# Kernel tuning notes

Measured on AMD Instinct MI355X. Metric: run time of the kernel, lower is better.

The kernel has to match this reference:

```python
import jax, jax.numpy as jnp
import numpy as np

K = 512   # codebook entries per group (num_embeddings // 4)
D = 128   # dim per group (embedding_dim // 4)
BETA = 0.25


def setup_inputs() -> dict:
    key = jax.random.key(0)
    k0, k1, k2, k3, k4 = jax.random.split(key, 5)
    latents = jax.random.normal(k0, (16, 2048, 512), dtype=jnp.float32)
    scale = 1.0 / K
    w1 = jax.random.uniform(k1, (K, D), dtype=jnp.float32, minval=-scale, maxval=scale)
    w2 = jax.random.uniform(k2, (K, D), dtype=jnp.float32, minval=-scale, maxval=scale)
    w3 = jax.random.uniform(k3, (K, D), dtype=jnp.float32, minval=-scale, maxval=scale)
    w4 = jax.random.uniform(k4, (K, D), dtype=jnp.float32, minval=-scale, maxval=scale)
    return {"latents": latents, "w1": w1, "w2": w2, "w3": w3, "w4": w4}


def _vq(latents, w1, w2, w3, w4):
    B, S, E = latents.shape
    # Slicing [:, :, g*D:(g+1)*D] is equivalent to reshape into groups.
    x = latents.reshape(B, S, 4, D)                    # [B,S,4,D]
    W = jnp.stack([w1, w2, w3, w4], axis=0)            # [4,K,D]
    x_sq = jnp.sum(x * x, axis=-1, keepdims=True)      # [B,S,4,1]
    w_sq = jnp.sum(W * W, axis=-1)                     # [4,K]
    cross = jnp.einsum('bsgd,gkd->bsgk', x, W)         # [B,S,4,K]
    dist = x_sq + w_sq[None, None, :, :] - 2.0 * cross
    idx = jnp.argmin(dist, axis=-1)                    # [B,S,4]
    g_idx = jnp.arange(4)[None, None, :]
    q = W[g_idx, idx]                                  # [B,S,4,D]
    # per-group MSE losses (mean over B,S,D)
    sg = jax.lax.stop_gradient
    commit = jnp.mean((sg(q) - x) ** 2, axis=(0, 1, 3))   # [4]
    embed = jnp.mean((q - sg(x)) ** 2, axis=(0, 1, 3))    # [4]
    vq_loss = jnp.sum(BETA * commit + embed)
    # straight-through estimator
    q_st = x + sg(q - x)
    return q_st.reshape(B, S, E), vq_loss


def reference(latents, w1, w2, w3, w4):
    return _vq(latents, w1, w2, w3, w4)
```

## Files before the change

### kernel.cpp

```cpp
#include <hip/hip_runtime.h>
#include <stdint.h>

typedef __attribute__((ext_vector_type(8))) short short8;
typedef __attribute__((ext_vector_type(4))) float f32x4;

#define BIG 4.0f

static __device__ __forceinline__ short f2bf(float f) {
    union { float f; uint32_t u; } v; v.f = f;
    uint32_t u = v.u;
    return (short)((u + 0x7FFFu + ((u >> 16) & 1u)) >> 16);
}

__global__ __launch_bounds__(512, 2)
void vq_main_kernel(const float* __restrict__ lat,
                    const float* __restrict__ w0, const float* __restrict__ w1,
                    const float* __restrict__ w2, const float* __restrict__ w3,
                    float* __restrict__ out, float* __restrict__ ws) {
    __shared__ __align__(16) short lw[65536];
    __shared__ float lwsq[512];
    __shared__ float slsum[8];

    const int bid   = blockIdx.x;
    const int g     = bid >> 6;
    const int tbase = (bid & 63) * 512;
    const float* wg = (g == 0) ? w0 : (g == 1) ? w1 : (g == 2) ? w2 : w3;

    const int t    = threadIdx.x;
    const int wave = t >> 6;
    const int l    = t & 63;
    const int lr   = l & 15;
    const int lh   = l >> 4;
    const int col  = (l & 31) * 4;
    const uint32_t invlr = 511 - lr;

    {
        const int cl = l & 15;
        const int ub = l >> 4;
        #pragma unroll
        for (int p = 0; p < 4; p++) {
            int c   = p * 128 + wave * 16 + cl;
            int nt2 = c >> 4;
            const float* src = wg + (size_t)c * 128;
            float s = 0.f;
            #pragma unroll
            for (int sp = 0; sp < 4; sp++) {
                int u   = ub + sp * 4;
                int ks2 = u >> 2, lh2 = u & 3;
                float4 v0 = *(const float4*)(src + u * 8);
                float4 v1 = *(const float4*)(src + u * 8 + 4);
                s += v0.x*v0.x + v0.y*v0.y + v0.z*v0.z + v0.w*v0.w
                   + v1.x*v1.x + v1.y*v1.y + v1.z*v1.z + v1.w*v1.w;
                short8 b;
                b[0] = f2bf(v0.x); b[1] = f2bf(v0.y); b[2] = f2bf(v0.z); b[3] = f2bf(v0.w);
                b[4] = f2bf(v1.x); b[5] = f2bf(v1.y); b[6] = f2bf(v1.z); b[7] = f2bf(v1.w);
                *(short8*)((char*)lw +
                    (size_t)(((nt2 * 4 + ks2) * 64 + lh2 * 16 + cl) * 16)) = b;
            }
            s += __shfl_xor(s, 16);
            s += __shfl_xor(s, 32);
            if (ub == 0) lwsq[c] = BIG - 0.5f * s;
        }
    }

    const char* lwb = (const char*)lw + l * 16;
    const int wtok = tbase + wave * 64;

    auto load_convert = [&](short8 (&fr)[2][4], float (&xsp)[2], int wt) {
        #pragma unroll
        for (int mt = 0; mt < 2; mt++) {
            int token = wt + mt * 16 + lr;
            const float* xp = lat + (size_t)token * 512 + g * 128 + lh * 8;
            float part = 0.f;
            #pragma unroll
            for (int ks = 0; ks < 4; ks++) {
                float4 v0 = *(const float4*)(xp + ks * 32);
                float4 v1 = *(const float4*)(xp + ks * 32 + 4);
                part += v0.x*v0.x + v0.y*v0.y + v0.z*v0.z + v0.w*v0.w
                      + v1.x*v1.x + v1.y*v1.y + v1.z*v1.z + v1.w*v1.w;
                short8 a;
                a[0] = f2bf(v0.x); a[1] = f2bf(v0.y); a[2] = f2bf(v0.z); a[3] = f2bf(v0.w);
                a[4] = f2bf(v1.x); a[5] = f2bf(v1.y); a[6] = f2bf(v1.z); a[7] = f2bf(v1.w);
                fr[mt][ks] = a;
            }
            part += __shfl_xor(part, 16);
            part += __shfl_xor(part, 32);
            xsp[mt] = part;
        }
    };

    auto compute = [&](short8 (&af)[2][4], uint32_t (&rk)[8]) {
        short8 p0 = *(const short8*)(lwb);
        short8 p1 = *(const short8*)(lwb + 1024);
        short8 p2 = *(const short8*)(lwb + 2048);
        short8 p3 = *(const short8*)(lwb + 3072);
        float  ph = lwsq[lr];
        #pragma unroll 4
        for (int nt = 0; nt < 32; nt++) {
            short8 c0 = p0, c1 = p1, c2 = p2, c3 = p3;
            float  hn = ph;
            const char* nb = lwb + ((nt + 1) & 31) * 4096;
            p0 = *(const short8*)(nb);
            p1 = *(const short8*)(nb + 1024);
            p2 = *(const short8*)(nb + 2048);
            p3 = *(const short8*)(nb + 3072);
            ph = lwsq[(((nt + 1) & 31) << 4) + lr];
            const uint32_t invc = invlr - (uint32_t)(nt * 16);
            __builtin_amdgcn_s_setprio(1);
            f32x4 acc0 = {hn, hn, hn, hn};
            f32x4 acc1 = {hn, hn, hn, hn};
            acc0 = __builtin_amdgcn_mfma_f32_16x16x32_bf16(af[0][0], c0, acc0, 0, 0, 0);
            acc0 = __builtin_amdgcn_mfma_f32_16x16x32_bf16(af[0][1], c1, acc0, 0, 0, 0);
            acc0 = __builtin_amdgcn_mfma_f32_16x16x32_bf16(af[0][2], c2, acc0, 0, 0, 0);
            acc0 = __builtin_amdgcn_mfma_f32_16x16x32_bf16(af[0][3], c3, acc0, 0, 0, 0);
            acc1 = __builtin_amdgcn_mfma_f32_16x16x32_bf16(af[1][0], c0, acc1, 0, 0, 0);
            acc1 = __builtin_amdgcn_mfma_f32_16x16x32_bf16(af[1][1], c1, acc1, 0, 0, 0);
            acc1 = __builtin_amdgcn_mfma_f32_16x16x32_bf16(af[1][2], c2, acc1, 0, 0, 0);
            acc1 = __builtin_amdgcn_mfma_f32_16x16x32_bf16(af[1][3], c3, acc1, 0, 0, 0);
            __builtin_amdgcn_s_setprio(0);
            #pragma unroll
            for (int r = 0; r < 4; r++) {
                rk[r]     = max(rk[r],     (__float_as_uint(acc0[r]) & 0xFFFFFE00u) | invc);
                rk[4 + r] = max(rk[4 + r], (__float_as_uint(acc1[r]) & 0xFFFFFE00u) | invc);
            }
        }
    };

    auto epilogue = [&](uint32_t (&rk)[8], float (&xsp)[2], int wt, float& acc_lsum) {
        int runidx[8];
        #pragma unroll
        for (int i = 0; i < 8; i++) {
            uint32_t k = rk[i];
            k = max(k, (uint32_t)__shfl_xor((int)k, 1));
            k = max(k, (uint32_t)__shfl_xor((int)k, 2));
            k = max(k, (uint32_t)__shfl_xor((int)k, 4));
            k = max(k, (uint32_t)__shfl_xor((int)k, 8));
            rk[i] = k;
            runidx[i] = 511 - (int)(k & 0x1FFu);
        }
        #pragma unroll
        for (int mt = 0; mt < 2; mt++) {
            #pragma unroll
            for (int r = 0; r < 4; r++) {
                int row = lh * 4 + r;
                float xs = __shfl(xsp[mt], (l & 48) | row);
                float val = __uint_as_float(rk[mt * 4 + r] & 0xFFFFFE00u);
                if (lr == 0) acc_lsum += xs + 2.f * BIG - 2.f * val;
            }
        }
        #pragma unroll
        for (int it = 0; it < 16; it++) {
            const int j0 = it * 2, j1 = it * 2 + 1;
            int idx0 = __shfl(runidx[((j0 >> 4) << 2) | (j0 & 3)], ((j0 >> 2) & 3) << 4);
            int idx1 = __shfl(runidx[((j1 >> 4) << 2) | (j1 & 3)], ((j1 >> 2) & 3) << 4);
            int idx  = (l >= 32) ? idx1 : idx0;
            int tloc = it * 2 + (l >> 5);
            float4 v = *(const float4*)(wg + (size_t)idx * 128 + col);
            *(float4*)(out + (size_t)(wt + tloc) * 512 + g * 128 + col) = v;
        }
    };

    short8 fA[2][4], fB[2][4];
    float  xspA[2], xspB[2];
    uint32_t kA[8], kB[8];
    #pragma unroll
    for (int i = 0; i < 8; i++) { kA[i] = 0u; kB[i] = 0u; }

    load_convert(fA, xspA, wtok);
    __syncthreads();

    float lsum = 0.f;
    compute(fA, kA);

    float4 raw[16];
    #pragma unroll
    for (int mt = 0; mt < 2; mt++) {
        #pragma unroll
        for (int ks = 0; ks < 4; ks++) {
            const float* xp = lat + (size_t)(wtok + 32 + mt * 16 + lr) * 512
                            + g * 128 + lh * 8 + ks * 32;
            raw[mt * 8 + ks * 2]     = *(const float4*)(xp);
            raw[mt * 8 + ks * 2 + 1] = *(const float4*)(xp + 4);
        }
    }

    int runidxA[8];
    #pragma unroll
    for (int i = 0; i < 8; i++) {
        uint32_t k = kA[i];
        k = max(k, (uint32_t)__shfl_xor((int)k, 1));
        k = max(k, (uint32_t)__shfl_xor((int)k, 2));
        k = max(k, (uint32_t)__shfl_xor((int)k, 4));
        k = max(k, (uint32_t)__shfl_xor((int)k, 8));
        kA[i] = k;
        runidxA[i] = 511 - (int)(k & 0x1FFu);
    }
    #pragma unroll
    for (int mt = 0; mt < 2; mt++) {
        #pragma unroll
        for (int r = 0; r < 4; r++) {
            int row = lh * 4 + r;
            float xs = __shfl(xspA[mt], (l & 48) | row);
            float val = __uint_as_float(kA[mt * 4 + r] & 0xFFFFFE00u);
            if (lr == 0) lsum += xs + 2.f * BIG - 2.f * val;
        }
    }
    int widx[16];
    #pragma unroll
    for (int it = 0; it < 16; it++) {
        const int j0 = it * 2, j1 = it * 2 + 1;
        int idx0 = __shfl(runidxA[((j0 >> 4) << 2) | (j0 & 3)], ((j0 >> 2) & 3) << 4);
        int idx1 = __shfl(runidxA[((j1 >> 4) << 2) | (j1 & 3)], ((j1 >> 2) & 3) << 4);
        widx[it] = (l >= 32) ? idx1 : idx0;
    }

    #pragma unroll
    for (int mt = 0; mt < 2; mt++) {
        float part = 0.f;
        #pragma unroll
        for (int ks = 0; ks < 4; ks++) {
            float4 v0 = raw[mt * 8 + ks * 2];
            float4 v1 = raw[mt * 8 + ks * 2 + 1];
            part += v0.x*v0.x + v0.y*v0.y + v0.z*v0.z + v0.w*v0.w
                  + v1.x*v1.x + v1.y*v1.y + v1.z*v1.z + v1.w*v1.w;
            short8 a;
            a[0] = f2bf(v0.x); a[1] = f2bf(v0.y); a[2] = f2bf(v0.z); a[3] = f2bf(v0.w);
            a[4] = f2bf(v1.x); a[5] = f2bf(v1.y); a[6] = f2bf(v1.z); a[7] = f2bf(v1.w);
            fB[mt][ks] = a;
        }
        part += __shfl_xor(part, 16);
        part += __shfl_xor(part, 32);
        xspB[mt] = part;
    }

    {
        short8 p0 = *(const short8*)(lwb);
        short8 p1 = *(const short8*)(lwb + 1024);
        short8 p2 = *(const short8*)(lwb + 2048);
        short8 p3 = *(const short8*)(lwb + 3072);
        float  ph = lwsq[lr];
        float4 vb0, vb1;

#define FUSED_NT(nt)                                                           \
        {                                                                      \
            short8 c0 = p0, c1 = p1, c2 = p2, c3 = p3;                         \
            float  hn = ph;                                                    \
            const char* nb = lwb + (((nt) + 1) & 31) * 4096;                   \
            p0 = *(const short8*)(nb);                                         \
            p1 = *(const short8*)(nb + 1024);                                  \
            p2 = *(const short8*)(nb + 2048);                                  \
            p3 = *(const short8*)(nb + 3072);                                  \
            ph = lwsq[((((nt) + 1) & 31) << 4) + lr];                          \
            const uint32_t invc = invlr - (uint32_t)((nt) * 16);               \
            __builtin_amdgcn_s_setprio(1);                                     \
            f32x4 acc0 = {hn, hn, hn, hn};                                     \
            f32x4 acc1 = {hn, hn, hn, hn};                                     \
            acc0 = __builtin_amdgcn_mfma_f32_16x16x32_bf16(fB[0][0], c0, acc0, 0, 0, 0); \
            acc0 = __builtin_amdgcn_mfma_f32_16x16x32_bf16(fB[0][1], c1, acc0, 0, 0, 0); \
            acc0 = __builtin_amdgcn_mfma_f32_16x16x32_bf16(fB[0][2], c2, acc0, 0, 0, 0); \
            acc0 = __builtin_amdgcn_mfma_f32_16x16x32_bf16(fB[0][3], c3, acc0, 0, 0, 0); \
            acc1 = __builtin_amdgcn_mfma_f32_16x16x32_bf16(fB[1][0], c0, acc1, 0, 0, 0); \
            acc1 = __builtin_amdgcn_mfma_f32_16x16x32_bf16(fB[1][1], c1, acc1, 0, 0, 0); \
            acc1 = __builtin_amdgcn_mfma_f32_16x16x32_bf16(fB[1][2], c2, acc1, 0, 0, 0); \
            acc1 = __builtin_amdgcn_mfma_f32_16x16x32_bf16(fB[1][3], c3, acc1, 0, 0, 0); \
            __builtin_amdgcn_s_setprio(0);                                     \
            kB[0] = max(kB[0], (__float_as_uint(acc0[0]) & 0xFFFFFE00u) | invc); \
            kB[1] = max(kB[1], (__float_as_uint(acc0[1]) & 0xFFFFFE00u) | invc); \
            kB[2] = max(kB[2], (__float_as_uint(acc0[2]) & 0xFFFFFE00u) | invc); \
            kB[3] = max(kB[3], (__float_as_uint(acc0[3]) & 0xFFFFFE00u) | invc); \
            kB[4] = max(kB[4], (__float_as_uint(acc1[0]) & 0xFFFFFE00u) | invc); \
            kB[5] = max(kB[5], (__float_as_uint(acc1[1]) & 0xFFFFFE00u) | invc); \
            kB[6] = max(kB[6], (__float_as_uint(acc1[2]) & 0xFFFFFE00u) | invc); \
            kB[7] = max(kB[7], (__float_as_uint(acc1[3]) & 0xFFFFFE00u) | invc); \
            if (((nt) & 3) == 1) {                                             \
                const int it0 = ((nt) >> 2) * 2;                               \
                vb0 = *(const float4*)(wg + (size_t)widx[it0] * 128 + col);    \
                vb1 = *(const float4*)(wg + (size_t)widx[it0 + 1] * 128 + col);\
            }                                                                  \
            if (((nt) & 3) == 3) {                                             \
                const int it0 = ((nt) >> 2) * 2;                               \
                *(float4*)(out + (size_t)(wtok + it0 * 2 + (l >> 5)) * 512     \
                           + g * 128 + col) = vb0;                             \
                *(float4*)(out + (size_t)(wtok + (it0 + 1) * 2 + (l >> 5)) * 512 \
                           + g * 128 + col) = vb1;                             \
            }                                                                  \
        }
#define FUSED_4(n) FUSED_NT(n) FUSED_NT((n) + 1) FUSED_NT((n) + 2) FUSED_NT((n) + 3)
        FUSED_4(0)  FUSED_4(4)  FUSED_4(8)  FUSED_4(12)
        FUSED_4(16) FUSED_4(20) FUSED_4(24) FUSED_4(28)
#undef FUSED_4
#undef FUSED_NT
    }

    epilogue(kB, xspB, wtok + 32, lsum);

    lsum += __shfl_xor(lsum, 16);
    lsum += __shfl_xor(lsum, 32);
    if (l == 0) slsum[wave] = lsum;
    __syncthreads();
    if (t == 0) {
        float s = 0.f;
        #pragma unroll
        for (int i = 0; i < 8; i++) s += slsum[i];
        ws[4096 + bid] = s;
    }
}

__global__ void vq_finalize_kernel(const float* __restrict__ ws, float* __restrict__ out) {
    __shared__ float s4[4];
    float v = ws[4096 + threadIdx.x];
    #pragma unroll
    for (int m = 1; m < 64; m <<= 1) v += __shfl_xor(v, m);
    if ((threadIdx.x & 63) == 0) s4[threadIdx.x >> 6] = v;
    __syncthreads();
    if (threadIdx.x == 0)
        out[16777216] = 1.25f * (s4[0] + s4[1] + s4[2] + s4[3]) * (1.0f / 4194304.0f);
}

extern "C" void kernel_launch(void* const* d_in, const int* in_sizes, int n_in,
                              void* d_out, int out_size, void* d_ws, size_t ws_size,
                              hipStream_t stream) {
    const float* lat = (const float*)d_in[0];
    const float* w1  = (const float*)d_in[1];
    const float* w2  = (const float*)d_in[2];
    const float* w3  = (const float*)d_in[3];
    const float* w4  = (const float*)d_in[4];
    float* out = (float*)d_out;
    float* ws  = (float*)d_ws;

    vq_main_kernel<<<256, 512, 0, stream>>>(lat, w1, w2, w3, w4, out, ws);
    vq_finalize_kernel<<<1, 256, 0, stream>>>(ws, out);
}
```

Before: 40.48 us.

## Interleave next tile's first-half latent loads and bf16 conversion into first MFMA loop

Replaces the compute lambda for tile A with a fully unrolled macro loop that, every 8 codebook tiles, issues global loads for one k-slice of the next tile's first 16 rows and converts them to bf16 a few iterations later. Only the second 16-row half is still loaded after the loop. The aim is to hide global-load latency and conversion ALU work behind the MFMA stream instead of stalling between tiles. The cost is higher register pressure from full unrolling and the extra in-flight float4 registers, which could hurt occupancy under launch_bounds(512,2).

```diff
diff --git a/kernel.cpp b/kernel.cpp
--- a/kernel.cpp
+++ b/kernel.cpp
@@ -89,43 +89,6 @@
         }
     };
 
-    auto compute = [&](short8 (&af)[2][4], uint32_t (&rk)[8]) {
-        short8 p0 = *(const short8*)(lwb);
-        short8 p1 = *(const short8*)(lwb + 1024);
-        short8 p2 = *(const short8*)(lwb + 2048);
-        short8 p3 = *(const short8*)(lwb + 3072);
-        float  ph = lwsq[lr];
-        #pragma unroll 4
-        for (int nt = 0; nt < 32; nt++) {
-            short8 c0 = p0, c1 = p1, c2 = p2, c3 = p3;
-            float  hn = ph;
-            const char* nb = lwb + ((nt + 1) & 31) * 4096;
-            p0 = *(const short8*)(nb);
-            p1 = *(const short8*)(nb + 1024);
-            p2 = *(const short8*)(nb + 2048);
-            p3 = *(const short8*)(nb + 3072);
-            ph = lwsq[(((nt + 1) & 31) << 4) + lr];
-            const uint32_t invc = invlr - (uint32_t)(nt * 16);
-            __builtin_amdgcn_s_setprio(1);
-            f32x4 acc0 = {hn, hn, hn, hn};
-            f32x4 acc1 = {hn, hn, hn, hn};
-            acc0 = __builtin_amdgcn_mfma_f32_16x16x32_bf16(af[0][0], c0, acc0, 0, 0, 0);
-            acc0 = __builtin_amdgcn_mfma_f32_16x16x32_bf16(af[0][1], c1, acc0, 0, 0, 0);
-            acc0 = __builtin_amdgcn_mfma_f32_16x16x32_bf16(af[0][2], c2, acc0, 0, 0, 0);
-            acc0 = __builtin_amdgcn_mfma_f32_16x16x32_bf16(af[0][3], c3, acc0, 0, 0, 0);
-            acc1 = __builtin_amdgcn_mfma_f32_16x16x32_bf16(af[1][0], c0, acc1, 0, 0, 0);
-            acc1 = __builtin_amdgcn_mfma_f32_16x16x32_bf16(af[1][1], c1, acc1, 0, 0, 0);
-            acc1 = __builtin_amdgcn_mfma_f32_16x16x32_bf16(af[1][2], c2, acc1, 0, 0, 0);
-            acc1 = __builtin_amdgcn_mfma_f32_16x16x32_bf16(af[1][3], c3, acc1, 0, 0, 0);
-            __builtin_amdgcn_s_setprio(0);
-            #pragma unroll
-            for (int r = 0; r < 4; r++) {
-                rk[r]     = max(rk[r],     (__float_as_uint(acc0[r]) & 0xFFFFFE00u) | invc);
-                rk[4 + r] = max(rk[4 + r], (__float_as_uint(acc1[r]) & 0xFFFFFE00u) | invc);
-            }
-        }
-    };
-
     auto epilogue = [&](uint32_t (&rk)[8], float (&xsp)[2], int wt, float& acc_lsum) {
         int runidx[8];
         #pragma unroll
@@ -162,25 +125,87 @@
 
     short8 fA[2][4], fB[2][4];
     float  xspA[2], xspB[2];
-    uint32_t kA[8], kB[8];
-    #pragma unroll
-    for (int i = 0; i < 8; i++) { kA[i] = 0u; kB[i] = 0u; }
+    uint32_t kA[8];
+    #pragma unroll
+    for (int i = 0; i < 8; i++) kA[i] = 0u;
 
     load_convert(fA, xspA, wtok);
     __syncthreads();
 
     float lsum = 0.f;
-    compute(fA, kA);
-
-    float4 raw[16];
-    #pragma unroll
-    for (int mt = 0; mt < 2; mt++) {
+    float xb0 = 0.f, xb1 = 0.f;
+
+    {
+        short8 p0 = *(const short8*)(lwb);
+        short8 p1 = *(const short8*)(lwb + 1024);
+        short8 p2 = *(const short8*)(lwb + 2048);
+        short8 p3 = *(const short8*)(lwb + 3072);
+        float  ph = lwsq[lr];
+        float4 rE0, rE1;
+
+#define CA_NT(nt)                                                              \
+        {                                                                      \
+            short8 c0 = p0, c1 = p1, c2 = p2, c3 = p3;                         \
+            float  hn = ph;                                                    \
+            const char* nb = lwb + (((nt) + 1) & 31) * 4096;                   \
+            p0 = *(const short8*)(nb);                                         \
+            p1 = *(const short8*)(nb + 1024);                                  \
+            p2 = *(const short8*)(nb + 2048);                                  \
+            p3 = *(const short8*)(nb + 3072);                                  \
+            ph = lwsq[((((nt) + 1) & 31) << 4) + lr];                          \
+            const uint32_t invc = invlr - (uint32_t)((nt) * 16);               \
+            __builtin_amdgcn_s_setprio(1);                                     \
+            f32x4 acc0 = {hn, hn, hn, hn};                                     \
+            f32x4 acc1 = {hn, hn, hn, hn};                                     \
+            acc0 = __builtin_amdgcn_mfma_f32_16x16x32_bf16(fA[0][0], c0, acc0, 0, 0, 0); \
+            acc0 = __builtin_amdgcn_mfma_f32_16x16x32_bf16(fA[0][1], c1, acc0, 0, 0, 0); \
+            acc0 = __builtin_amdgcn_mfma_f32_16x16x32_bf16(fA[0][2], c2, acc0, 0, 0, 0); \
+            acc0 = __builtin_amdgcn_mfma_f32_16x16x32_bf16(fA[0][3], c3, acc0, 0, 0, 0); \
+            acc1 = __builtin_amdgcn_mfma_f32_16x16x32_bf16(fA[1][0], c0, acc1, 0, 0, 0); \
+            acc1 = __builtin_amdgcn_mfma_f32_16x16x32_bf16(fA[1][1], c1, acc1, 0, 0, 0); \
+            acc1 = __builtin_amdgcn_mfma_f32_16x16x32_bf16(fA[1][2], c2, acc1, 0, 0, 0); \
+            acc1 = __builtin_amdgcn_mfma_f32_16x16x32_bf16(fA[1][3], c3, acc1, 0, 0, 0); \
+            __builtin_amdgcn_s_setprio(0);                                     \
+            kA[0] = max(kA[0], (__float_as_uint(acc0[0]) & 0xFFFFFE00u) | invc); \
+            kA[1] = max(kA[1], (__float_as_uint(acc0[1]) & 0xFFFFFE00u) | invc); \
+            kA[2] = max(kA[2], (__float_as_uint(acc0[2]) & 0xFFFFFE00u) | invc); \
+            kA[3] = max(kA[3], (__float_as_uint(acc0[3]) & 0xFFFFFE00u) | invc); \
+            kA[4] = max(kA[4], (__float_as_uint(acc1[0]) & 0xFFFFFE00u) | invc); \
+            kA[5] = max(kA[5], (__float_as_uint(acc1[1]) & 0xFFFFFE00u) | invc); \
+            kA[6] = max(kA[6], (__float_as_uint(acc1[2]) & 0xFFFFFE00u) | invc); \
+            kA[7] = max(kA[7], (__float_as_uint(acc1[3]) & 0xFFFFFE00u) | invc); \
+            if (((nt) & 7) == 0) {                                             \
+                const int bks = (nt) >> 3;                                     \
+                const float* xp = lat + (size_t)(wtok + 32 + lr) * 512         \
+                                + g * 128 + lh * 8 + bks * 32;                 \
+                rE0 = *(const float4*)(xp);                                    \
+                rE1 = *(const float4*)(xp + 4);                                \
+            }                                                                  \
+            if (((nt) & 7) == 6) {                                             \
+                const int bks = (nt) >> 3;                                     \
+                float ss = rE0.x*rE0.x + rE0.y*rE0.y + rE0.z*rE0.z + rE0.w*rE0.w \
+                         + rE1.x*rE1.x + rE1.y*rE1.y + rE1.z*rE1.z + rE1.w*rE1.w; \
+                xb0 += ss;                                                     \
+                short8 a;                                                      \
+                a[0] = f2bf(rE0.x); a[1] = f2bf(rE0.y); a[2] = f2bf(rE0.z); a[3] = f2bf(rE0.w); \
+                a[4] = f2bf(rE1.x); a[5] = f2bf(rE1.y); a[6] = f2bf(rE1.z); a[7] = f2bf(rE1.w); \
+                fB[0][bks] = a;                                                \
+            }                                                                  \
+        }
+#define CA_4(n) CA_NT(n) CA_NT((n) + 1) CA_NT((n) + 2) CA_NT((n) + 3)
+        CA_4(0)  CA_4(4)  CA_4(8)  CA_4(12)
+        CA_4(16) CA_4(20) CA_4(24) CA_4(28)
+#undef CA_4
+#undef CA_NT
+    }
+
+    float4 raw[8];
+    {
+        const float* xp = lat + (size_t)(wtok + 48 + lr) * 512 + g * 128 + lh * 8;
         #pragma unroll
         for (int ks = 0; ks < 4; ks++) {
-            const float* xp = lat + (size_t)(wtok + 32 + mt * 16 + lr) * 512
-                            + g * 128 + lh * 8 + ks * 32;
-            raw[mt * 8 + ks * 2]     = *(const float4*)(xp);
-            raw[mt * 8 + ks * 2 + 1] = *(const float4*)(xp + 4);
+            raw[ks * 2]     = *(const float4*)(xp + ks * 32);
+            raw[ks * 2 + 1] = *(const float4*)(xp + ks * 32 + 4);
         }
     }
 
@@ -215,23 +240,26 @@
     }
 
     #pragma unroll
-    for (int mt = 0; mt < 2; mt++) {
-        float part = 0.f;
-        #pragma unroll
-        for (int ks = 0; ks < 4; ks++) {
-            float4 v0 = raw[mt * 8 + ks * 2];
-            float4 v1 = raw[mt * 8 + ks * 2 + 1];
-            part += v0.x*v0.x + v0.y*v0.y + v0.z*v0.z + v0.w*v0.w
-                  + v1.x*v1.x + v1.y*v1.y + v1.z*v1.z + v1.w*v1.w;
-            short8 a;
-            a[0] = f2bf(v0.x); a[1] = f2bf(v0.y); a[2] = f2bf(v0.z); a[3] = f2bf(v0.w);
-            a[4] = f2bf(v1.x); a[5] = f2bf(v1.y); a[6] = f2bf(v1.z); a[7] = f2bf(v1.w);
-            fB[mt][ks] = a;
-        }
-        part += __shfl_xor(part, 16);
-        part += __shfl_xor(part, 32);
-        xspB[mt] = part;
-    }
+    for (int ks = 0; ks < 4; ks++) {
+        float4 v0 = raw[ks * 2];
+        float4 v1 = raw[ks * 2 + 1];
+        xb1 += v0.x*v0.x + v0.y*v0.y + v0.z*v0.z + v0.w*v0.w
+             + v1.x*v1.x + v1.y*v1.y + v1.z*v1.z + v1.w*v1.w;
+        short8 a;
+        a[0] = f2bf(v0.x); a[1] = f2bf(v0.y); a[2] = f2bf(v0.z); a[3] = f2bf(v0.w);
+        a[4] = f2bf(v1.x); a[5] = f2bf(v1.y); a[6] = f2bf(v1.z); a[7] = f2bf(v1.w);
+        fB[1][ks] = a;
+    }
+    xb0 += __shfl_xor(xb0, 16);
+    xb0 += __shfl_xor(xb0, 32);
+    xb1 += __shfl_xor(xb1, 16);
+    xb1 += __shfl_xor(xb1, 32);
+    xspB[0] = xb0;
+    xspB[1] = xb1;
+
+    uint32_t kB[8];
+    #pragma unroll
+    for (int i = 0; i < 8; i++) kB[i] = 0u;
 
     {
         short8 p0 = *(const short8*)(lwb);
```

Measured after the change: 68.50 us. +69.2%, slower.
